# Performance work log

Hardware: AMD Instinct MI355X
Metric: run time of the kernel (lower is better)

Reference implementation:

```python
import jax, jax.numpy as jnp
import numpy as np

NUM_TREES = 100
TREE_DEPTH = 5
INPUT_DIM = 256
NUM_CLASSES = 64
BATCH = 8192
NUM_NODES = 2 ** TREE_DEPTH - 1   # 31 decision nodes per tree
NUM_LEAVES = 2 ** TREE_DEPTH      # 32 leaves per tree


def setup_inputs() -> dict:
    key = jax.random.key(0)
    k_x, k_w, k_b, k_l = jax.random.split(key, 4)
    x = jax.random.normal(k_x, (BATCH, INPUT_DIM), dtype=jnp.float32)
    # stacked per-tree decision-node params (torch.randn init)
    node_w = jax.random.normal(k_w, (NUM_TREES, NUM_NODES, INPUT_DIM), dtype=jnp.float32)
    node_b = jax.random.normal(k_b, (NUM_TREES, NUM_NODES), dtype=jnp.float32)
    leaves = jax.random.normal(k_l, (NUM_TREES, NUM_LEAVES, NUM_CLASSES), dtype=jnp.float32)
    return {"x": x, "node_w": node_w, "node_b": node_b, "leaves": leaves}


def reference(x, node_w, node_b, leaves):
    # x: [B, D]; node_w: [T, Nn, D]; node_b: [T, Nn]; leaves: [T, Nl, C]
    T = node_w.shape[0]
    B = x.shape[0]
    depth = int(np.log2(leaves.shape[1]))
    idx = jnp.zeros((T, B), dtype=jnp.int32)
    for _ in range(depth):  # small fixed depth loop
        # gather each sample's routing node per tree: [T, B, D] and [T, B]
        w_g = jnp.take_along_axis(node_w, idx[:, :, None], axis=1)
        b_g = jnp.take_along_axis(node_b, idx, axis=1)
        decisions = jax.nn.sigmoid(jnp.einsum('tbd,bd->tb', w_g, x) + b_g)
        idx = 2 * idx + (decisions <= 0.5).astype(jnp.int32)
    # leaf gather: [T, B, C], then forest average over trees -> [B, C]
    tree_preds = jnp.take_along_axis(leaves, idx[:, :, None], axis=1)
    return jnp.mean(tree_preds, axis=0)
```

## Files before the change

### kernel.cpp

```cpp
#include <hip/hip_runtime.h>


typedef __bf16 bf16;
typedef __attribute__((ext_vector_type(8))) __bf16 bf16x8;
typedef __attribute__((ext_vector_type(4))) float f32x4;

#define NTREES 100
#define NB     8192
#define ND     256
#define NNODES 31
#define NLEAF  32
#define NCLS   64
#define TAU    2.0e-3f

static __device__ __forceinline__ int traverse(const float z[16], float* mn_out) {
    float a0 = z[0];
    bool d0 = a0 <= 0.f;
    float a1 = d0 ? z[1] : z[0];
    bool d1 = a1 <= 0.f;
    float a2 = d0 ? (d1 ? z[3] : z[2]) : (d1 ? z[1] : z[0]);
    bool d2 = a2 <= 0.f;
    float m0 = d2 ? z[1] : z[0], m1 = d2 ? z[3] : z[2];
    float m2 = d2 ? z[5] : z[4], m3 = d2 ? z[7] : z[6];
    float p0 = d1 ? m1 : m0, p1 = d1 ? m3 : m2;
    float a3 = d0 ? p1 : p0;
    bool d3 = a3 <= 0.f;
    float n0 = d3 ? z[1] : z[0],  n1 = d3 ? z[3] : z[2];
    float n2 = d3 ? z[5] : z[4],  n3 = d3 ? z[7] : z[6];
    float n4 = d3 ? z[9] : z[8],  n5 = d3 ? z[11] : z[10];
    float n6 = d3 ? z[13] : z[12], n7 = d3 ? z[15] : z[14];
    float q0 = d2 ? n1 : n0, q1 = d2 ? n3 : n2;
    float q2 = d2 ? n5 : n4, q3 = d2 ? n7 : n6;
    float r0 = d1 ? q1 : q0, r1 = d1 ? q3 : q2;
    float a4 = d0 ? r1 : r0;
    bool d4 = a4 <= 0.f;
    *mn_out = fminf(fminf(fminf(fabsf(a0), fabsf(a1)),
                          fminf(fabsf(a2), fabsf(a3))), fabsf(a4));
    return ((int)d0 << 4) | ((int)d1 << 3) | ((int)d2 << 2)
         | ((int)d3 << 1) | (int)d4;
}

__global__ __launch_bounds__(256, 2) void forest_all(
    const float* __restrict__ x,
    const float* __restrict__ wf,
    const float* __restrict__ bias,
    unsigned char* __restrict__ idxb)
{
    __shared__ char lds[65536];

    const int tid  = threadIdx.x;
    const int wave = tid >> 6;
    const int lane = tid & 63;
    const int m    = lane & 15;
    const int q    = lane >> 4;

    const int lin  = blockIdx.x + gridDim.x * blockIdx.y;
    const int xcd  = lin & 7;
    const int slot = lin >> 3;
    const int mg   = xcd * 4 + (slot / 13);
    const int tg   = slot % 13;

    f32x4 acc[4][8];
#pragma unroll
    for (int mi = 0; mi < 4; ++mi)
#pragma unroll
        for (int ni = 0; ni < 8; ++ni)
            acc[mi][ni] = (f32x4){0.f, 0.f, 0.f, 0.f};

    const float* xbase = x + (size_t)(mg * 256 + wave * 64 + m) * ND + q * 8;

    auto stage = [&](int kq, char* buf) {
#pragma unroll
        for (int it = 0; it < 4; ++it) {
            int idx = it * 256 + tid;
            int oct = idx & 7, row = idx >> 3;
            int tree = tg * 8 + (row >> 4), node = row & 15;
            f32x4 v0 = (f32x4){0.f, 0.f, 0.f, 0.f};
            f32x4 v1 = (f32x4){0.f, 0.f, 0.f, 0.f};
            if (tree < NTREES) {
                const float* src = wf + ((size_t)tree * NNODES + node) * ND
                                 + kq * 64 + oct * 8;
                v0 = *(const f32x4*)src;
                v1 = *(const f32x4*)(src + 4);
            }
            bf16x8 h8, l8;
#pragma unroll
            for (int e = 0; e < 4; ++e) {
                bf16 h0 = (bf16)v0[e];
                h8[e]     = h0; l8[e]     = (bf16)(v0[e] - (float)h0);
                bf16 h1 = (bf16)v1[e];
                h8[4 + e] = h1; l8[4 + e] = (bf16)(v1[e] - (float)h1);
            }
            int cp = oct ^ (row & 7);
            bf16* dst = (bf16*)buf + row * 64 + cp * 8;
            *(bf16x8*)dst = h8;
            *(bf16x8*)(dst + 8192) = l8;
        }
    };

    stage(0, lds);
    f32x4 raw[4][2];
#pragma unroll
    for (int mi = 0; mi < 4; ++mi) {
        raw[mi][0] = *(const f32x4*)(xbase + mi * 4096);
        raw[mi][1] = *(const f32x4*)(xbase + mi * 4096 + 4);
    }
    __syncthreads();

    bf16x8 cah[4], cal[4];
#pragma unroll
    for (int kq = 0; kq < 4; ++kq) {
        const bf16* bufc = (const bf16*)(lds + (kq & 1) * 32768);
        if (kq < 3) stage(kq + 1, lds + ((kq + 1) & 1) * 32768);
#pragma unroll
        for (int kkq = 0; kkq < 2; ++kkq) {
            const int kk = kq * 2 + kkq;
#pragma unroll
            for (int mi = 0; mi < 4; ++mi) {
#pragma unroll
                for (int e = 0; e < 4; ++e) {
                    float f0 = raw[mi][0][e], f1 = raw[mi][1][e];
                    bf16 h0 = (bf16)f0, h1 = (bf16)f1;
                    cah[mi][e]     = h0; cal[mi][e]     = (bf16)(f0 - (float)h0);
                    cah[mi][4 + e] = h1; cal[mi][4 + e] = (bf16)(f1 - (float)h1);
                }
            }
            if (kk < 7) {
#pragma unroll
                for (int mi = 0; mi < 4; ++mi) {
                    raw[mi][0] = *(const f32x4*)(xbase + mi * 4096 + (kk + 1) * 32);
                    raw[mi][1] = *(const f32x4*)(xbase + mi * 4096 + (kk + 1) * 32 + 4);
                }
            }
#pragma unroll
            for (int ni = 0; ni < 8; ++ni) {
                const int n  = ni * 16 + m;
                const int cp = (kkq * 4 + q) ^ (m & 7);
                bf16x8 bh = *(const bf16x8*)(bufc + n * 64 + cp * 8);
                bf16x8 bl = *(const bf16x8*)(bufc + 8192 + n * 64 + cp * 8);
#pragma unroll
                for (int mi = 0; mi < 4; ++mi) {
                    acc[mi][ni] = __builtin_amdgcn_mfma_f32_16x16x32_bf16(cal[mi], bh, acc[mi][ni], 0, 0, 0);
                    acc[mi][ni] = __builtin_amdgcn_mfma_f32_16x16x32_bf16(cah[mi], bl, acc[mi][ni], 0, 0, 0);
                    acc[mi][ni] = __builtin_amdgcn_mfma_f32_16x16x32_bf16(cah[mi], bh, acc[mi][ni], 0, 0, 0);
                }
            }
        }
        __syncthreads();
    }

    float biasv[8];
#pragma unroll
    for (int ni = 0; ni < 8; ++ni) {
        int tree = tg * 8 + ni;
        biasv[ni] = (tree < NTREES) ? bias[(size_t)tree * NNODES + m] : 0.f;
    }

    float* ws_ = (float*)lds + wave * 1280;
    const int sg = mg * 256 + wave * 64 + lane;
    unsigned int pk0 = 0, pk1 = 0;
#pragma unroll
    for (int ni = 0; ni < 8; ++ni) {
#pragma unroll
        for (int mi = 0; mi < 4; ++mi)
#pragma unroll
            for (int r = 0; r < 4; ++r)
                ws_[(mi * 16 + q * 4 + r) * 20 + m] = acc[mi][ni][r] + biasv[ni];
        f32x4 z0 = *(f32x4*)&ws_[lane * 20];
        f32x4 z1 = *(f32x4*)&ws_[lane * 20 + 4];
        f32x4 z2 = *(f32x4*)&ws_[lane * 20 + 8];
        f32x4 z3 = *(f32x4*)&ws_[lane * 20 + 12];
        float z[16] = {z0[0], z0[1], z0[2], z0[3], z1[0], z1[1], z1[2], z1[3],
                       z2[0], z2[1], z2[2], z2[3], z3[0], z3[1], z3[2], z3[3]};
        float mn;
        int leaf = traverse(z, &mn);
        const int tree = tg * 8 + ni;
        if (tree < NTREES && mn < TAU) {
            const float* xr = x + (size_t)sg * ND;
            float zc[16];
#pragma unroll
            for (int nd = 0; nd < 16; ++nd) zc[nd] = z[nd];
#pragma unroll
            for (int nd = 0; nd < 16; ++nd) {
                if (fabsf(z[nd]) < TAU) {
                    const float* wr = wf + ((size_t)tree * NNODES + nd) * ND;
                    double s0 = 0.0, s1 = 0.0;
#pragma unroll 4
                    for (int k2 = 0; k2 < 32; ++k2) {
                        f32x4 xv = *(const f32x4*)(xr + k2 * 8);
                        f32x4 wv = *(const f32x4*)(wr + k2 * 8);
                        f32x4 xu = *(const f32x4*)(xr + k2 * 8 + 4);
                        f32x4 wu = *(const f32x4*)(wr + k2 * 8 + 4);
                        s0 += (double)xv[0] * wv[0] + (double)xv[1] * wv[1]
                            + (double)xv[2] * wv[2] + (double)xv[3] * wv[3];
                        s1 += (double)xu[0] * wu[0] + (double)xu[1] * wu[1]
                            + (double)xu[2] * wu[2] + (double)xu[3] * wu[3];
                    }
                    double zt = s0 + s1 + (double)bias[(size_t)tree * NNODES + nd];
                    zc[nd] = (zt <= 0.0) ? -1.f : 1.f;
                }
            }
            float mn2;
            leaf = traverse(zc, &mn2);
        }
        if (ni < 4) pk0 |= (unsigned)leaf << (8 * ni);
        else        pk1 |= (unsigned)leaf << (8 * (ni - 4));
    }
    unsigned char* dst = idxb + (size_t)sg * NTREES + tg * 8;
    *(unsigned int*)dst = pk0;
    if (tg < 12) *(unsigned int*)(dst + 4) = pk1;
}

__global__ void leaf_gather(const unsigned char* __restrict__ idxb,
                            const float* __restrict__ lv,
                            float* __restrict__ out) {
    const int wave = threadIdx.x >> 6;
    const int lane = threadIdx.x & 63;
    const int s = blockIdx.x * 4 + wave;
    unsigned int rw = 0;
    if (lane < 25) rw = *(const unsigned int*)(idxb + (size_t)s * NTREES + lane * 4);
    float acc = 0.f;
#pragma unroll 10
    for (int t = 0; t < NTREES; ++t) {
        unsigned int wrd = __shfl(rw, t >> 2);
        int li = (wrd >> ((t & 3) * 8)) & 255;
        acc += lv[((size_t)t * NLEAF + li) * NCLS + lane];
    }
    out[(size_t)s * NCLS + lane] = acc * 0.01f;
}

extern "C" void kernel_launch(void* const* d_in, const int* in_sizes, int n_in,
                              void* d_out, int out_size, void* d_ws, size_t ws_size,
                              hipStream_t stream) {
    const float* x  = (const float*)d_in[0];
    const float* nw = (const float*)d_in[1];
    const float* nb = (const float*)d_in[2];
    const float* lv = (const float*)d_in[3];
    float* out = (float*)d_out;

    unsigned char* idxb = (unsigned char*)d_ws;
    if (ws_size < (size_t)NB * NTREES) return;

    forest_all<<<dim3(13, 32), 256, 0, stream>>>(x, nw, nb, idxb);
    leaf_gather<<<NB / 4, 256, 0, stream>>>(idxb, lv, out);
}
```

Measured before the change: 111.1 us.

## Pre-split weights into swizzled bf16 image and stream via global_load_lds

Adds a prep kernel that converts node weights once into a pre-swizzled hi/lo bf16 LDS image. The main kernel then fills LDS with direct global-to-LDS loads instead of having every block reload fp32 and convert. The x hi/lo split now uses bit masks and byte permutes instead of conversion instructions. Leaves are also converted to bf16 for the gather kernel, which halves gather bytes but adds rounding error to the output and costs an extra launch.

```diff
diff --git a/kernel.cpp b/kernel.cpp
--- a/kernel.cpp
+++ b/kernel.cpp
@@ -4,6 +4,7 @@
 typedef __bf16 bf16;
 typedef __attribute__((ext_vector_type(8))) __bf16 bf16x8;
 typedef __attribute__((ext_vector_type(4))) float f32x4;
+typedef __attribute__((ext_vector_type(4))) unsigned int u32x4;
 
 #define NTREES 100
 #define NB     8192
@@ -12,6 +13,35 @@
 #define NLEAF  32
 #define NCLS   64
 #define TAU    2.0e-3f
+
+static __device__ __forceinline__ void gload16(const void* g, void* l) {
+    __builtin_amdgcn_global_load_lds(
+        (const __attribute__((address_space(1))) void*)g,
+        (__attribute__((address_space(3))) void*)l, 16, 0, 0);
+}
+
+static __device__ __forceinline__ void split8(const f32x4 v0, const f32x4 v1,
+                                              bf16x8* hi, bf16x8* lo) {
+    u32x4 b0 = __builtin_bit_cast(u32x4, v0);
+    u32x4 b1 = __builtin_bit_cast(u32x4, v1);
+    u32x4 h0 = b0 & 0xFFFF0000u;
+    u32x4 h1 = b1 & 0xFFFF0000u;
+    f32x4 r0 = v0 - __builtin_bit_cast(f32x4, h0);
+    f32x4 r1 = v1 - __builtin_bit_cast(f32x4, h1);
+    u32x4 c0 = __builtin_bit_cast(u32x4, r0);
+    u32x4 c1 = __builtin_bit_cast(u32x4, r1);
+    u32x4 hp, lp;
+    hp[0] = __builtin_amdgcn_perm(b0[1], b0[0], 0x07060302u);
+    hp[1] = __builtin_amdgcn_perm(b0[3], b0[2], 0x07060302u);
+    hp[2] = __builtin_amdgcn_perm(b1[1], b1[0], 0x07060302u);
+    hp[3] = __builtin_amdgcn_perm(b1[3], b1[2], 0x07060302u);
+    lp[0] = __builtin_amdgcn_perm(c0[1], c0[0], 0x07060302u);
+    lp[1] = __builtin_amdgcn_perm(c0[3], c0[2], 0x07060302u);
+    lp[2] = __builtin_amdgcn_perm(c1[1], c1[0], 0x07060302u);
+    lp[3] = __builtin_amdgcn_perm(c1[3], c1[2], 0x07060302u);
+    *hi = __builtin_bit_cast(bf16x8, hp);
+    *lo = __builtin_bit_cast(bf16x8, lp);
+}
 
 static __device__ __forceinline__ int traverse(const float z[16], float* mn_out) {
     float a0 = z[0];
@@ -40,8 +70,41 @@
          | ((int)d3 << 1) | (int)d4;
 }
 
+__global__ void prep(const float* __restrict__ wf, const float* __restrict__ lv,
+                     bf16* __restrict__ wimg, bf16* __restrict__ lv16) {
+    if (blockIdx.x < 208) {
+        int i = blockIdx.x * 256 + threadIdx.x;
+        int oct_g = i & 31;
+        int row   = (i >> 5) & 127;
+        int tg    = i >> 12;
+        int tree  = tg * 8 + (row >> 4), node = row & 15;
+        bf16x8 h8, l8;
+        if (tree < NTREES) {
+            const float* src = wf + ((size_t)tree * NNODES + node) * ND + oct_g * 8;
+#pragma unroll
+            for (int e = 0; e < 8; ++e) {
+                float f = src[e];
+                bf16 h = (bf16)f;
+                h8[e] = h;
+                l8[e] = (bf16)(f - (float)h);
+            }
+        } else {
+#pragma unroll
+            for (int e = 0; e < 8; ++e) { h8[e] = (bf16)0.f; l8[e] = (bf16)0.f; }
+        }
+        int kq = oct_g >> 3, oct = oct_g & 7, cp = oct ^ (row & 7);
+        size_t b = (size_t)tg * 65536 + (size_t)kq * 16384 + row * 64 + cp * 8;
+        *(bf16x8*)(wimg + b)        = h8;
+        *(bf16x8*)(wimg + b + 8192) = l8;
+    } else {
+        int i = (blockIdx.x - 208) * 256 + threadIdx.x;
+        lv16[i] = (bf16)lv[i];
+    }
+}
+
 __global__ __launch_bounds__(256, 2) void forest_all(
     const float* __restrict__ x,
+    const bf16* __restrict__ wimg,
     const float* __restrict__ wf,
     const float* __restrict__ bias,
     unsigned char* __restrict__ idxb)
@@ -68,37 +131,13 @@
             acc[mi][ni] = (f32x4){0.f, 0.f, 0.f, 0.f};
 
     const float* xbase = x + (size_t)(mg * 256 + wave * 64 + m) * ND + q * 8;
-
-    auto stage = [&](int kq, char* buf) {
-#pragma unroll
-        for (int it = 0; it < 4; ++it) {
-            int idx = it * 256 + tid;
-            int oct = idx & 7, row = idx >> 3;
-            int tree = tg * 8 + (row >> 4), node = row & 15;
-            f32x4 v0 = (f32x4){0.f, 0.f, 0.f, 0.f};
-            f32x4 v1 = (f32x4){0.f, 0.f, 0.f, 0.f};
-            if (tree < NTREES) {
-                const float* src = wf + ((size_t)tree * NNODES + node) * ND
-                                 + kq * 64 + oct * 8;
-                v0 = *(const f32x4*)src;
-                v1 = *(const f32x4*)(src + 4);
-            }
-            bf16x8 h8, l8;
-#pragma unroll
-            for (int e = 0; e < 4; ++e) {
-                bf16 h0 = (bf16)v0[e];
-                h8[e]     = h0; l8[e]     = (bf16)(v0[e] - (float)h0);
-                bf16 h1 = (bf16)v1[e];
-                h8[4 + e] = h1; l8[4 + e] = (bf16)(v1[e] - (float)h1);
-            }
-            int cp = oct ^ (row & 7);
-            bf16* dst = (bf16*)buf + row * 64 + cp * 8;
-            *(bf16x8*)dst = h8;
-            *(bf16x8*)(dst + 8192) = l8;
-        }
-    };
-
-    stage(0, lds);
+    const bf16* wsrc = wimg + (size_t)tg * 65536;
+
+#pragma unroll
+    for (int j = 0; j < 8; ++j) {
+        int idx = j * 256 + tid;
+        gload16(wsrc + idx * 8, lds + idx * 16);
+    }
     f32x4 raw[4][2];
 #pragma unroll
     for (int mi = 0; mi < 4; ++mi) {
@@ -107,24 +146,24 @@
     }
     __syncthreads();
 
-    bf16x8 cah[4], cal[4];
 #pragma unroll
     for (int kq = 0; kq < 4; ++kq) {
         const bf16* bufc = (const bf16*)(lds + (kq & 1) * 32768);
-        if (kq < 3) stage(kq + 1, lds + ((kq + 1) & 1) * 32768);
+        if (kq < 3) {
+            char* bufn = lds + ((kq + 1) & 1) * 32768;
+#pragma unroll
+            for (int j = 0; j < 8; ++j) {
+                int idx = j * 256 + tid;
+                gload16(wsrc + (size_t)(kq + 1) * 16384 + idx * 8, bufn + idx * 16);
+            }
+        }
 #pragma unroll
         for (int kkq = 0; kkq < 2; ++kkq) {
             const int kk = kq * 2 + kkq;
-#pragma unroll
-            for (int mi = 0; mi < 4; ++mi) {
-#pragma unroll
-                for (int e = 0; e < 4; ++e) {
-                    float f0 = raw[mi][0][e], f1 = raw[mi][1][e];
-                    bf16 h0 = (bf16)f0, h1 = (bf16)f1;
-                    cah[mi][e]     = h0; cal[mi][e]     = (bf16)(f0 - (float)h0);
-                    cah[mi][4 + e] = h1; cal[mi][4 + e] = (bf16)(f1 - (float)h1);
-                }
-            }
+            bf16x8 cah[4], cal[4];
+#pragma unroll
+            for (int mi = 0; mi < 4; ++mi)
+                split8(raw[mi][0], raw[mi][1], &cah[mi], &cal[mi]);
             if (kk < 7) {
 #pragma unroll
                 for (int mi = 0; mi < 4; ++mi) {
@@ -212,7 +251,7 @@
 }
 
 __global__ void leaf_gather(const unsigned char* __restrict__ idxb,
-                            const float* __restrict__ lv,
+                            const bf16* __restrict__ lv16,
                             float* __restrict__ out) {
     const int wave = threadIdx.x >> 6;
     const int lane = threadIdx.x & 63;
@@ -224,7 +263,7 @@
     for (int t = 0; t < NTREES; ++t) {
         unsigned int wrd = __shfl(rw, t >> 2);
         int li = (wrd >> ((t & 3) * 8)) & 255;
-        acc += lv[((size_t)t * NLEAF + li) * NCLS + lane];
+        acc += (float)lv16[((size_t)t * NLEAF + li) * NCLS + lane];
     }
     out[(size_t)s * NCLS + lane] = acc * 0.01f;
 }
@@ -238,9 +277,13 @@
     const float* lv = (const float*)d_in[3];
     float* out = (float*)d_out;
 
-    unsigned char* idxb = (unsigned char*)d_ws;
-    if (ws_size < (size_t)NB * NTREES) return;
-
-    forest_all<<<dim3(13, 32), 256, 0, stream>>>(x, nw, nb, idxb);
-    leaf_gather<<<NB / 4, 256, 0, stream>>>(idxb, lv, out);
-}
+    char* ws = (char*)d_ws;
+    bf16* wimg = (bf16*)(ws + 0);
+    unsigned char* idxb = (unsigned char*)(ws + 1703936);
+    bf16* lv16 = (bf16*)(ws + 2523136);
+    if (ws_size < (size_t)2932736) return;
+
+    prep<<<1008, 256, 0, stream>>>(nw, lv, wimg, lv16);
+    forest_all<<<dim3(13, 32), 256, 0, stream>>>(x, wimg, nw, nb, idxb);
+    leaf_gather<<<NB / 4, 256, 0, stream>>>(idxb, lv16, out);
+}
```

Result: slower. 118.8 us (+6.9%).
